# Optimization experiments

Measured on AMD Instinct MI355X. Metric: run time of the kernel, lower is better.

## Reference

```python
import jax, jax.numpy as jnp
import numpy as np

B, NS, NC, D = 32, 1024, 1024, 256   # batch, sentence len, comment len, latent/embedding dim
K = 128                              # co-attention latent size (self.k)
CLIP_R = 2.0
EPS = 1e-5

def _norm(x):
    return jnp.sqrt(jnp.maximum(jnp.sum(x * x, -1, keepdims=True), 1e-15))

def artanh(x):
    x = jnp.clip(x, -1 + 1e-5, 1 - 1e-5)
    return 0.5 * (jnp.log1p(x) - jnp.log1p(-x))

# ---------- Poincare ball, c = 1 ----------
def p_logmap0(y):
    yn = _norm(y)
    return artanh(yn) * y / yn

def p_expmap0(u):
    un = _norm(u)
    return jnp.tanh(un) * u / un

def mobius_add(x, y):
    xy = jnp.sum(x * y, -1, keepdims=True)
    x2 = jnp.sum(x * x, -1, keepdims=True)
    y2 = jnp.sum(y * y, -1, keepdims=True)
    num = (1 + 2 * xy + y2) * x + (1 - x2) * y
    den = jnp.maximum(1 + 2 * xy + x2 * y2, 1e-15)
    return num / den

def mobius_matvec(m, x):
    # geoopt convention: result = 'x @ m^T' transported through the ball
    xn = _norm(x)
    mx = jnp.matmul(x, jnp.swapaxes(m, -1, -2))
    mxn = _norm(mx)
    return jnp.tanh(mxn / xn * artanh(xn)) * mx / mxn

# ---------- Lorentz hyperboloid, k = 1 ----------
def l_expmap0_space(v_space):
    # exp map at origin of a tangent vector with zero time component
    vn = _norm(v_space)
    return jnp.concatenate([jnp.cosh(vn), jnp.sinh(vn) * v_space / vn], -1)

def euclid_to_lorentz(x):
    xn = _norm(x) + EPS
    x = x * jnp.minimum(1.0, CLIP_R / xn)  # clip_r feature clipping
    return l_expmap0_space(x)              # F.pad time=0 then expmap0

def lorentz_linear(x, W, b):
    y = jnp.matmul(x, W.T) + b
    space = y[..., 1:]
    time = jnp.sqrt(jnp.sum(space * space, -1, keepdims=True) + 1.0)
    return jnp.concatenate([time, space], -1)

def lorentz_act(x):
    space = jax.nn.gelu(x[..., 1:], approximate=False)
    time = jnp.sqrt(jnp.sum(space * space, -1, keepdims=True) + 1.0)
    return jnp.concatenate([time, space], -1)

def lorentz_to_poincare(x):
    return x[..., 1:] / (x[..., :1] + 1.0)

def l_inner(u, v):
    return -u[..., :1] * v[..., :1] + jnp.sum(u[..., 1:] * v[..., 1:], -1, keepdims=True)

def centroid(x, w):
    avg = jnp.matmul(w, x)  # weighted Lorentz average, then renormalize to hyperboloid
    den = jnp.sqrt(jnp.maximum(jnp.abs(l_inner(avg, avg)), 1e-8))
    return avg / den

def l_logmap0_space(x):
    t = jnp.maximum(x[..., :1], 1 + 1e-7)
    return jnp.arccosh(t) * x[..., 1:] / _norm(x[..., 1:])

def lorentz_concat(x, y):
    z = jnp.concatenate([l_logmap0_space(x), l_logmap0_space(y)], -1)
    return l_expmap0_space(z)


def setup_inputs() -> dict:
    key = jax.random.key(0)
    ks = jax.random.split(key, 8)
    sentence = jax.random.normal(ks[0], (B, NS, D), jnp.float32)
    comment = jax.random.normal(ks[1], (B, NC, D), jnp.float32)
    comment = 0.9 * comment / (_norm(comment) + 1.0)  # valid Poincare-ball points
    w = lambda k, o, i: jax.random.normal(k, (o, i), jnp.float32) * 0.05
    return {
        'sentence_rep': sentence,
        'comment_rep': comment,
        'Wl_W': w(ks[2], D + 1, D + 1), 'Wl_b': jnp.zeros((D + 1,), jnp.float32),
        'Wc_W': w(ks[3], K + 1, D + 1), 'Wc_b': jnp.zeros((K + 1,), jnp.float32),
        'Ws_W': w(ks[4], K + 1, D + 1), 'Ws_b': jnp.zeros((K + 1,), jnp.float32),
        'whs': jax.random.uniform(ks[5], (1, K), jnp.float32),
        'whc': jax.random.uniform(ks[6], (1, K), jnp.float32),
    }


def reference(sentence_rep, comment_rep, Wl_W, Wl_b, Wc_W, Wc_b, Ws_W, Ws_b, whs, whc):
    T = lambda a: jnp.swapaxes(a, -1, -2)
    # Fourier mixing (real part, as torch .float() on complex)
    s = jnp.fft.fft2(sentence_rep).real.astype(jnp.float32)
    c = jnp.fft.fft2(p_logmap0(comment_rep)).real.astype(jnp.float32)
    Ls = euclid_to_lorentz(s)            # [B,NS,D+1]
    Lc = euclid_to_lorentz(c)            # [B,NC,D+1]
    L = lorentz_linear(Lc, Wl_W, Wl_b)   # [B,NC,D+1]
    L = lorentz_act(jnp.einsum('bnd,bmd->bnm', Ls, L))  # [B,NS,NC] affinity
    # Ws(sentence) and Wc(comment) in Poincare coords (computed once; original recomputes)
    Hs_a = lorentz_to_poincare(lorentz_linear(Ls, Ws_W, Ws_b))  # [B,NS,K]
    Hc_a = lorentz_to_poincare(lorentz_linear(Lc, Wc_W, Wc_b))  # [B,NC,K]
    Hs_b = mobius_matvec(T(Hc_a), L)          # [B,NS,K]
    Hs = mobius_add(Hs_a, Hs_b)
    Hs = p_expmap0(jax.nn.gelu(p_logmap0(Hs), approximate=False))
    Hc_b = mobius_matvec(T(Hs_a), T(L))       # [B,NC,K]
    Hc = mobius_add(T(Hc_a), T(Hc_b))         # [B,K,NC]
    Hc = p_expmap0(jax.nn.gelu(p_logmap0(Hc), approximate=False))
    As = jax.nn.softmax(T(mobius_matvec(whs, Hs)), axis=-1)     # [B,1,NS]
    Ac = jax.nn.softmax(T(mobius_matvec(whc, T(Hc))), axis=-1)  # [B,1,NC]
    co_s = centroid(Ls, As)                   # [B,1,D+1]
    co_c = centroid(Lc, Ac)                   # [B,1,D+1]
    co_sc = jnp.squeeze(lorentz_concat(co_s, co_c), axis=1)     # [B,2D+1]
    return co_sc, As, Ac
```

## Files before the change

### kernel.cpp

```cpp
#include <hip/hip_runtime.h>
#include <cstdint>
#include <math.h>

#define NBATCH 32
#define NSQ 1024
#define NCQ 1024
#define DDIM 256
#define DP 257
#define KQ 128
#define KPAD 288
#define NFOLD 640
#define KF2 640
#define MXSPLIT 4194304

typedef __attribute__((ext_vector_type(8))) short short8;
typedef __attribute__((ext_vector_type(4))) float floatx4;

__device__ __forceinline__ float bf2f(ushort u) { return __uint_as_float(((uint)u) << 16); }
__device__ __forceinline__ ushort f2bf(float f) {
    uint u = __float_as_uint(f);
    return (ushort)((u + 0x7FFFu + ((u >> 16) & 1u)) >> 16);
}
__device__ __forceinline__ void gload16(const void* g, void* l) {
    __builtin_amdgcn_global_load_lds(
        (const __attribute__((address_space(1))) void*)g,
        (__attribute__((address_space(3))) void*)l,
        16, 0, 0);
}
__device__ __forceinline__ float artanh_clip(float x) {
    x = fminf(fmaxf(x, -1.0f + 1e-5f), 1.0f - 1e-5f);
    return 0.5f * (log1pf(x) - log1pf(-x));
}
__device__ __forceinline__ float gelu_f(float x) {
    return 0.5f * x * (1.0f + erff(x * 0.70710678118654752440f));
}
__device__ __forceinline__ float waveRedSum(float v) {
#pragma unroll
    for (int o = 32; o > 0; o >>= 1) v += __shfl_down(v, o, 64);
    return __shfl(v, 0, 64);
}
__device__ __forceinline__ void waveRedSum3(float& a, float& b, float& c) {
#pragma unroll
    for (int o = 32; o > 0; o >>= 1) {
        a += __shfl_down(a, o, 64);
        b += __shfl_down(b, o, 64);
        c += __shfl_down(c, o, 64);
    }
    a = __shfl(a, 0, 64); b = __shfl(b, 0, 64); c = __shfl(c, 0, 64);
}
__device__ __forceinline__ void waveRedSum2(float& a, float& b) {
#pragma unroll
    for (int o = 32; o > 0; o >>= 1) {
        a += __shfl_down(a, o, 64);
        b += __shfl_down(b, o, 64);
    }
    a = __shfl(a, 0, 64); b = __shfl(b, 0, 64);
}
__device__ __forceinline__ float blockRedSum(float v, float* buf) {
    int lane = threadIdx.x & 63, wid = threadIdx.x >> 6;
#pragma unroll
    for (int o = 32; o > 0; o >>= 1) v += __shfl_down(v, o, 64);
    __syncthreads();
    if (lane == 0) buf[wid] = v;
    __syncthreads();
    int nw = blockDim.x >> 6;
    float s = buf[0];
    for (int i = 1; i < nw; i++) s += buf[i];
    return s;
}
__device__ __forceinline__ float blockRedMax(float v, float* buf) {
    int lane = threadIdx.x & 63, wid = threadIdx.x >> 6;
#pragma unroll
    for (int o = 32; o > 0; o >>= 1) v = fmaxf(v, __shfl_down(v, o, 64));
    __syncthreads();
    if (lane == 0) buf[wid] = v;
    __syncthreads();
    int nw = blockDim.x >> 6;
    float s = buf[0];
    for (int i = 1; i < nw; i++) s = fmaxf(s, buf[i]);
    return s;
}

template <bool OUT_BF16, bool BIAS, bool ATOMIC, int NSPLIT, bool DUAL>
__global__ __launch_bounds__(256) void mfma_gemm(
    const short* __restrict__ A, int lda, int64_t sA,
    const short* __restrict__ B, int ldb, int64_t sB,
    void* __restrict__ Cv, int ldc, int64_t sC,
    const float* __restrict__ bias, int M, int N, int K,
    const short* __restrict__ A1, const short* __restrict__ B1, int64_t cOff1,
    const float* __restrict__ biasB)
{
    __shared__ short As0[128][32];
    __shared__ short Bs0[128][32];
    __shared__ short As1[128][32];
    __shared__ short Bs1[128][32];
    int bx = blockIdx.x, by = blockIdx.y, bz = blockIdx.z;
    {
        const int gx = gridDim.x, gy = gridDim.y;
        const int nblk = gx * gy * gridDim.z;
        if ((nblk & 7) == 0) {
            int flat = bx + gx * (by + gy * bz);
            int logical = (flat & 7) * (nblk >> 3) + (flat >> 3);
            bx = logical % gx; logical /= gx;
            by = logical % gy; bz = logical / gy;
        }
    }
    const int zz = bz;
    int zb, ks, half;
    if (DUAL) { half = zz & 1; zb = zz >> 1; ks = 0; }
    else      { zb = zz / NSPLIT; ks = zz - zb * NSPLIT; half = 0; }
    const short* Ap = (DUAL && half) ? A1 : A;
    const short* Bp = (DUAL && half) ? B1 : B;
    Ap += (int64_t)zb * sA;
    Bp += (int64_t)zb * sB;
    const int kper = K / NSPLIT;
    const int kbeg = ks * kper, kend = kbeg + kper;
    const int m0 = by * 128, n0 = bx * 128;
    const int t = threadIdx.x;
    const int lane = t & 63, w = t >> 6;
    const int wm = (w & 1) * 64, wn = (w >> 1) * 64;
    const int sr = t >> 2, sc8 = (t & 3) * 8;
    floatx4 acc[4][4] = {};

    auto stageA = [&](short (*S)[32], int kk) {
        const short* ap = Ap + (int64_t)(m0 + sr) * lda + kk + sc8;
        gload16(ap, &S[sr][sc8]);
        gload16(ap + (int64_t)64 * lda, &S[sr + 64][sc8]);
    };
    auto stageB = [&](short (*S)[32], int kk) {
        const short* bp = Bp + (int64_t)(n0 + sr) * ldb + kk + sc8;
        gload16(bp, &S[sr][sc8]);
        gload16(bp + (int64_t)64 * ldb, &S[sr + 64][sc8]);
    };
    auto domfma = [&](short (*SA)[32], short (*SB)[32]) {
        short8 af[4], bfv[4];
#pragma unroll
        for (int i = 0; i < 4; i++)
            af[i] = *(const short8*)&SA[wm + 16 * i + (lane & 15)][8 * (lane >> 4)];
#pragma unroll
        for (int i = 0; i < 4; i++)
            bfv[i] = *(const short8*)&SB[wn + 16 * i + (lane & 15)][8 * (lane >> 4)];
#pragma unroll
        for (int i = 0; i < 4; i++)
#pragma unroll
            for (int j = 0; j < 4; j++)
                acc[i][j] = __builtin_amdgcn_mfma_f32_16x16x32_bf16(af[i], bfv[j], acc[i][j], 0, 0, 0);
    };

    int k0 = kbeg;
    for (; k0 + 64 <= kend; k0 += 64) {
        stageA(As0, k0);       stageB(Bs0, k0);
        stageA(As1, k0 + 32);  stageB(Bs1, k0 + 32);
        __syncthreads();
        domfma(As0, Bs0);
        domfma(As1, Bs1);
        __syncthreads();
    }
    if (k0 < kend) {
        stageA(As0, k0);      stageB(Bs0, k0);
        __syncthreads();
        domfma(As0, Bs0);
        __syncthreads();
    }

    const int q = lane >> 4, c = lane & 15;
    int64_t cbase = (int64_t)zb * sC + ((DUAL && half) ? cOff1 : 0);
    if (NSPLIT > 1 && !ATOMIC) cbase += (int64_t)ks * cOff1;
    const float* bsel = (BIAS && biasB && zb) ? biasB : bias;
#pragma unroll
    for (int j = 0; j < 4; j++) {
        int col = n0 + wn + 16 * j + c;
        float bv = BIAS ? bsel[col] : 0.0f;
#pragma unroll
        for (int i = 0; i < 4; i++) {
            int rowb = m0 + wm + 16 * i + 4 * q;
#pragma unroll
            for (int r = 0; r < 4; r++) {
                float v = acc[i][j][r] + bv;
                int64_t idx = cbase + (int64_t)(rowb + r) * ldc + col;
                if (ATOMIC)       atomicAdd((float*)Cv + idx, v);
                else if (OUT_BF16) ((ushort*)Cv)[idx] = f2bf(v);
                else               ((float*)Cv)[idx] = v;
            }
        }
    }
}

__global__ __launch_bounds__(256) void trigtab_kernel(float* __restrict__ tab) {
    int p = blockIdx.x * 256 + threadIdx.x;
    float ang = (6.28318530717958647692f / 1024.0f) * (float)p;
    tab[p] = cosf(ang);
    tab[1024 + p] = sinf(ang);
}

__global__ __launch_bounds__(256) void genconst_kernel(
    const float* __restrict__ tab,
    ushort* CS1c, ushort* CS1s, ushort* C2, ushort* S2,
    const float* __restrict__ WlW, const float* __restrict__ WsW, const float* __restrict__ WcW,
    ushort* Wl, ushort* Ws, ushort* Wc)
{
    __shared__ float lct[1024], lst[1024];
    int blk = blockIdx.x, t = threadIdx.x;
    if (blk < 704) {
        for (int i = t; i < 1024; i += 256) { lct[i] = tab[i]; lst[i] = tab[1024 + i]; }
        __syncthreads();
    }
    if (blk < 640) {
        int n = blk;
        for (int k = t; k < 544; k += 256) {
            float vc, vs;
            if (k <= 512) {
                int p = (n * k) & 1023;
                vc = lct[p];
                vs = (k == 0) ? 0.0f : -lst[p];
            } else { vc = 0.0f; vs = 0.0f; }
            CS1c[n * KF2 + k] = f2bf(vc);
            CS1s[n * KF2 + k] = f2bf(vs);
        }
    } else if (blk < 704) {
        int base = (blk - 640) * 1024;
#pragma unroll
        for (int i = 0; i < 4; i++) {
            int idx = base + t + 256 * i;
            int d = idx >> 8, j = idx & 255;
            int p = ((d * j) & 255) << 2;
            C2[idx] = f2bf(lct[p]);
            S2[idx] = f2bf(lst[p]);
        }
    } else {
        int r = blk - 704;
        const float* src; ushort* dst; int srow;
        if (r < 256)      { src = WlW; dst = Wl + r * KPAD;        srow = r + 1; }
        else if (r < 384) { src = WsW; dst = Ws + (r - 256) * KPAD; srow = r - 256 + 1; }
        else              { src = WcW; dst = Wc + (r - 384) * KPAD; srow = r - 384 + 1; }
        dst[t] = (t < DP) ? f2bf(src[(int64_t)srow * DP + t]) : (ushort)0;
        if (t < KPAD - 256) {
            int t2 = t + 256;
            dst[t2] = (t2 < DP) ? f2bf(src[(int64_t)srow * DP + t2]) : (ushort)0;
        }
    }
}

__global__ __launch_bounds__(256) void prep_fold_kernel(const float* __restrict__ sent,
                                                        const float* __restrict__ comm,
                                                        ushort* __restrict__ XC, ushort* __restrict__ XS) {
    int bp = blockIdx.x;
    int z = blockIdx.y * 4 + (threadIdx.x >> 6);
    int lane = threadIdx.x & 63;
    int m2 = (1024 - bp) & 1023;
    const float* base = (z < 32) ? sent + (int64_t)z * 262144 : comm + (int64_t)(z - 32) * 262144;
    float4 a = *(const float4*)(base + bp * 256 + 4 * lane);
    float4 b = *(const float4*)(base + m2 * 256 + 4 * lane);
    if (z >= 32) {
        float s1 = a.x * a.x + a.y * a.y + a.z * a.z + a.w * a.w;
        float s2 = b.x * b.x + b.y * b.y + b.z * b.z + b.w * b.w;
        waveRedSum2(s1, s2);
        float yn1 = sqrtf(fmaxf(s1, 1e-15f));
        float f1 = artanh_clip(yn1) / yn1;
        a.x *= f1; a.y *= f1; a.z *= f1; a.w *= f1;
        float yn2 = sqrtf(fmaxf(s2, 1e-15f));
        float f2v = artanh_clip(yn2) / yn2;
        b.x *= f2v; b.y *= f2v; b.z *= f2v; b.w *= f2v;
    }
    int64_t o = ((int64_t)z * NFOLD + bp) * 256 + 4 * lane;
    bool single = (bp == 0) || (bp == 512);
    ushort4 oc;
    oc.x = f2bf(single ? a.x : a.x + b.x);
    oc.y = f2bf(single ? a.y : a.y + b.y);
    oc.z = f2bf(single ? a.z : a.z + b.z);
    oc.w = f2bf(single ? a.w : a.w + b.w);
    *(ushort4*)(XC + o) = oc;
    if (!single) {
        ushort4 os;
        os.x = f2bf(a.x - b.x); os.y = f2bf(a.y - b.y);
        os.z = f2bf(a.z - b.z); os.w = f2bf(a.w - b.w);
        *(ushort4*)(XS + o) = os;
    }
}

__global__ __launch_bounds__(256) void e2l_kernel(const ushort* __restrict__ YcYs,
                                                  ushort* __restrict__ Lsb, ushort* __restrict__ Lcb) {
    int64_t row = (int64_t)blockIdx.x * 4 + (threadIdx.x >> 6);
    int lane = threadIdx.x & 63;
    int z = (int)(row >> 10), n = (int)(row & 1023);
    int np = (n <= 512) ? n : 1024 - n;
    float sgn = (n <= 512) ? 1.0f : -1.0f;
    const ushort* base = YcYs + (int64_t)z * 327680 + np * 256 + 4 * lane;
    ushort4 uc = *(const ushort4*)base;
    ushort4 us = *(const ushort4*)(base + 163840);
    float v0 = bf2f(uc.x) + sgn * bf2f(us.x);
    float v1 = bf2f(uc.y) + sgn * bf2f(us.y);
    float v2 = bf2f(uc.z) + sgn * bf2f(us.z);
    float v3 = bf2f(uc.w) + sgn * bf2f(us.w);
    float s = waveRedSum(v0 * v0 + v1 * v1 + v2 * v2 + v3 * v3);
    float xn = sqrtf(fmaxf(s, 1e-15f)) + 1e-5f;
    float sc = fminf(1.0f, 2.0f / xn);
    float s2 = fmaxf(s * sc * sc, 1e-15f);
    float vn = sqrtf(s2);
    float e = expf(vn);
    float ei = 1.0f / e;
    float shv = (vn < 1e-4f) ? 1.0f : (e - ei) * 0.5f / vn;
    float fac = shv * sc;
    ushort* ob = (row < 32768 ? Lsb + row * KPAD : Lcb + (row - 32768) * KPAD);
    ob[1 + 4 * lane + 0] = f2bf(fac * v0);
    ob[1 + 4 * lane + 1] = f2bf(fac * v1);
    ob[1 + 4 * lane + 2] = f2bf(fac * v2);
    ob[1 + 4 * lane + 3] = f2bf(fac * v3);
    if (lane == 0) ob[0] = f2bf((e + ei) * 0.5f);
    if (lane < KPAD - DP) ob[DP + lane] = 0;
}

__global__ __launch_bounds__(256) void lnorm_kernel(ushort* __restrict__ Llin_bf) {
    int64_t row = (int64_t)blockIdx.x * 4 + (threadIdx.x >> 6);
    int lane = threadIdx.x & 63;
    ushort* ob = Llin_bf + row * KPAD;
    float s = 0.f;
#pragma unroll
    for (int i = 0; i < 4; i++) { float v = bf2f(ob[1 + 4 * lane + i]); s += v * v; }
    s = waveRedSum(s);
    if (lane == 0) ob[0] = f2bf(sqrtf(s + 1.0f));
    if (lane < KPAD - DP) ob[DP + lane] = 0;
}

__global__ __launch_bounds__(256) void poinc2_kernel(ushort* __restrict__ Hcat) {
    int64_t row = (int64_t)blockIdx.x * 4 + (threadIdx.x >> 6);
    int lane = threadIdx.x & 63;
    ushort* r = Hcat + row * KQ;
    ushort2 u = *(ushort2*)&r[2 * lane];
    float v0 = bf2f(u.x), v1 = bf2f(u.y);
    float s = waveRedSum(v0 * v0 + v1 * v1);
    float inv = 1.0f / (sqrtf(s + 1.0f) + 1.0f);
    ushort2 o; o.x = f2bf(v0 * inv); o.y = f2bf(v1 * inv);
    *(ushort2*)&r[2 * lane] = o;
}

__global__ __launch_bounds__(256) void tmat_kernel(ushort* __restrict__ inout, ushort* __restrict__ outp,
                                                   float* __restrict__ rowpart, float* __restrict__ colpart) {
    __shared__ ushort tile[64][68];
    int z = blockIdx.z;
    int r0 = blockIdx.x * 64, c0 = blockIdx.y * 64;
    ushort* ib = inout + (int64_t)z * 1048576;
    ushort* ob = outp + (int64_t)z * 1048576;
    int t = threadIdx.x;
    int row = t >> 2;
    int cq = (t & 3) * 8;
    {
        ushort* src = ib + (int64_t)(r0 + row) * 1024 + c0;
        float rsum = 0.f;
#pragma unroll
        for (int s = 0; s < 2; s++) {
            int cb = cq + 32 * s;
            uint4 v = *(const uint4*)(src + cb);
            ushort g[8];
            const ushort* pv = (const ushort*)&v;
#pragma unroll
            for (int k = 0; k < 8; k++) {
                g[k] = f2bf(gelu_f(bf2f(pv[k])));
                float fb = bf2f(g[k]);
                if (!(c0 == 0 && cb == 0 && k == 0)) rsum += fb * fb;
            }
            *(uint4*)(src + cb) = *(const uint4*)g;
            *(ushort4*)&tile[row][cb] = *(const ushort4*)&g[0];
            *(ushort4*)&tile[row][cb + 4] = *(const ushort4*)&g[4];
        }
        rsum += __shfl_xor(rsum, 1, 64);
        rsum += __shfl_xor(rsum, 2, 64);
        if ((t & 3) == 0)
            rowpart[((int64_t)(z * 16 + blockIdx.y)) * 1024 + r0 + row] = rsum;
    }
    __syncthreads();
    {
        int i2 = row;
        ushort* dst = ob + (int64_t)(c0 + i2) * 1024 + r0;
        float csum = 0.f;
#pragma unroll
        for (int s = 0; s < 2; s++) {
            int cb = cq + 32 * s;
            ushort g[8];
#pragma unroll
            for (int k = 0; k < 8; k++) {
                g[k] = tile[cb + k][i2];
                float a = bf2f(g[k]);
                csum += a * a;
            }
            *(uint4*)(dst + cb) = *(const uint4*)g;
        }
        csum += __shfl_xor(csum, 1, 64);
        csum += __shfl_xor(csum, 2, 64);
        if ((t & 3) == 0)
            colpart[((int64_t)(z * 16 + blockIdx.x)) * 1024 + c0 + i2] = csum;
    }
}

__global__ __launch_bounds__(256) void combine_kernel(
    const float* __restrict__ rowpart, const float* __restrict__ colpart,
    ushort* __restrict__ Lmat, ushort* __restrict__ LmatT,
    float* __restrict__ xnrow, float* __restrict__ colsum)
{
    __shared__ float red[4];
    int b = blockIdx.x, t = threadIdx.x;
    float t2 = 0.f;
#pragma unroll
    for (int i = 0; i < 4; i++) {
        int n = t + 256 * i;
        const float* rp = rowpart + (int64_t)b * 16384 + n;
        float s = 0.f;
#pragma unroll
        for (int c = 0; c < 16; c++) s += rp[c * 1024];
        float tim = sqrtf(1.0f + s);
        ushort tb = f2bf(tim);
        Lmat[((int64_t)(b * 1024 + n)) * 1024] = tb;
        LmatT[(int64_t)b * 1048576 + n] = tb;
        xnrow[b * 1024 + n] = sqrtf(fmaxf(1.0f + 2.0f * s, 1e-15f));
        t2 += tim * tim;
    }
#pragma unroll
    for (int i = 0; i < 4; i++) {
        int m = t + 256 * i;
        const float* cp = colpart + (int64_t)b * 16384 + m;
        float s = 0.f;
#pragma unroll
        for (int c = 0; c < 16; c++) s += cp[c * 1024];
        if (m > 0) colsum[b * 1024 + m] = s;
    }
    float tt = blockRedSum(t2, red);
    if (t == 0) colsum[b * 1024] = tt;
}

__global__ __launch_bounds__(256) void colfac_kernel(const float* __restrict__ colsum,
                                                     const float* __restrict__ mxcT,
                                                     float* __restrict__ fac_c) {
    int b = blockIdx.x; int m = blockIdx.y * 256 + threadIdx.x;
    float xn = sqrtf(fmaxf(colsum[b * NCQ + m], 1e-15f));
    const float* base = mxcT + (int64_t)b * KQ * NCQ + m;
    const float* base2 = base + MXSPLIT;
    float sm = 0.f;
    for (int j = 0; j < KQ; j++) {
        float v = base[j * NCQ] + base2[j * NCQ];
        sm += v * v;
    }
    float mxn = sqrtf(fmaxf(sm, 1e-15f));
    fac_c[b * NCQ + m] = tanhf(mxn / xn * artanh_clip(xn)) / mxn;
}

__global__ __launch_bounds__(256) void rowops_s_kernel(
    const ushort* __restrict__ Hsa, const float* __restrict__ mxs,
    const float* __restrict__ xnrow, const float* __restrict__ whs,
    float* __restrict__ logits)
{
    const int t = threadIdx.x;
    const int lane = t & 63;
    const int wid = t >> 6;
    const int sub = lane & 7;
    const int rg  = lane >> 3;
    const int64_t row = (int64_t)blockIdx.x * 32 + wid * 8 + rg;
    const ushort* p = Hsa + row * KQ + sub * 16;
    const float*  q = mxs + row * KQ + sub * 16;

    float pf[16], qf[16];
    {
        uint4 u0 = *(const uint4*)p;
        uint4 u1 = *(const uint4*)(p + 8);
        const ushort* pu0 = (const ushort*)&u0;
        const ushort* pu1 = (const ushort*)&u1;
#pragma unroll
        for (int i = 0; i < 8; i++) { pf[i] = bf2f(pu0[i]); pf[8 + i] = bf2f(pu1[i]); }
    }
#pragma unroll
    for (int i = 0; i < 16; i += 4) {
        float4 a  = *(const float4*)(q + i);
        float4 b2 = *(const float4*)(q + i + MXSPLIT);
        qf[i + 0] = a.x + b2.x; qf[i + 1] = a.y + b2.y;
        qf[i + 2] = a.z + b2.z; qf[i + 3] = a.w + b2.w;
    }
    float r1 = 0.f, r2 = 0.f, r3 = 0.f;
#pragma unroll
    for (int i = 0; i < 16; i++) {
        r1 += qf[i] * qf[i]; r2 += pf[i] * qf[i]; r3 += pf[i] * pf[i];
    }
#pragma unroll
    for (int o = 4; o > 0; o >>= 1) {
        r1 += __shfl_xor(r1, o, 64);
        r2 += __shfl_xor(r2, o, 64);
        r3 += __shfl_xor(r3, o, 64);
    }
    float mxn = sqrtf(fmaxf(r1, 1e-15f));
    float xn = xnrow[row];
    float fac = tanhf(mxn / xn * artanh_clip(xn)) / mxn;
    float xy = fac * r2;
    float x2 = r3;
    float y2 = fac * fac * r1;
    float ca = 1.f + 2.f * xy + y2, cb = 1.f - x2;
    float den = fmaxf(1.f + 2.f * xy + x2 * y2, 1e-15f);
    float hn2 = (ca * ca * x2 + 2.f * ca * cb * xy + cb * cb * y2) / (den * den);
    float hn = sqrtf(fmaxf(hn2, 1e-15f));
    float uf = artanh_clip(hn) / hn;
    float ufd = uf / den;
    float cbf = cb * fac;
    float wv[16];
#pragma unroll
    for (int i = 0; i < 16; i += 4) *(float4*)&wv[i] = *(const float4*)(whs + sub * 16 + i);
    float r4 = 0.f, r5 = 0.f;
#pragma unroll
    for (int i = 0; i < 16; i++) {
        float g = gelu_f(ufd * (ca * pf[i] + cbf * qf[i]));
        r4 += g * g;
        r5 += g * wv[i];
    }
#pragma unroll
    for (int o = 4; o > 0; o >>= 1) {
        r4 += __shfl_xor(r4, o, 64);
        r5 += __shfl_xor(r5, o, 64);
    }
    float gn = sqrtf(fmaxf(r4, 1e-15f));
    float ef = tanhf(gn) / gn;
    float dot = ef * r5;
    float Hn = sqrtf(fmaxf(ef * ef * r4, 1e-15f));
    float mxn2 = sqrtf(fmaxf(dot * dot, 1e-15f));
    float lg = tanhf(mxn2 / Hn * artanh_clip(Hn)) * dot / mxn2;
    if (sub == 0) logits[row] = lg;
}

__global__ void thsa_kernel(const ushort* __restrict__ in, ushort* __restrict__ outp) {
    __shared__ ushort tile[32][33];
    int z = blockIdx.z;
    int n0 = blockIdx.x * 32, j0 = blockIdx.y * 32;
    const ushort* ib = in + (int64_t)z * 131072;
    ushort* ob = outp + (int64_t)z * 131072;
    int tx = threadIdx.x, ty = threadIdx.y;
    for (int i = 0; i < 32; i += 8) tile[ty + i][tx] = ib[(n0 + ty + i) * 128 + j0 + tx];
    __syncthreads();
    for (int i = 0; i < 32; i += 8) ob[(j0 + ty + i) * 1024 + n0 + tx] = tile[tx][ty + i];
}

__global__ __launch_bounds__(256) void rowops_c_kernel(const ushort* __restrict__ HcAT,
                                                       float* __restrict__ mx,
                                                       const float* __restrict__ fac_c) {
    int64_t row = (int64_t)blockIdx.x * 4 + (threadIdx.x >> 6);
    int lane = threadIdx.x & 63;
    int b = (int)(row >> 7);
    const ushort* xb = HcAT + row * (int64_t)NCQ + 16 * lane;
    float* yb = mx + row * (int64_t)NCQ + 16 * lane;
    const float* fb = fac_c + b * NCQ + 16 * lane;
    float xv[16], yv[16];
    {
        uint4 u0 = *(const uint4*)xb;
        uint4 u1 = *(const uint4*)(xb + 8);
        const ushort* pu0 = (const ushort*)&u0;
        const ushort* pu1 = (const ushort*)&u1;
#pragma unroll
        for (int i = 0; i < 8; i++) { xv[i] = bf2f(pu0[i]); xv[8 + i] = bf2f(pu1[i]); }
    }
#pragma unroll
    for (int i = 0; i < 16; i += 4) {
        float4 v1 = *(const float4*)(yb + i);
        float4 v2 = *(const float4*)(yb + i + MXSPLIT);
        float4 fv = *(const float4*)(fb + i);
        yv[i + 0] = fv.x * (v1.x + v2.x);
        yv[i + 1] = fv.y * (v1.y + v2.y);
        yv[i + 2] = fv.z * (v1.z + v2.z);
        yv[i + 3] = fv.w * (v1.w + v2.w);
    }
    float xy = 0.f, x2 = 0.f, y2 = 0.f;
#pragma unroll
    for (int i = 0; i < 16; i++) { xy += xv[i] * yv[i]; x2 += xv[i] * xv[i]; y2 += yv[i] * yv[i]; }
    waveRedSum3(xy, x2, y2);
    float ca = 1.f + 2.f * xy + y2, cb = 1.f - x2;
    float den = fmaxf(1.f + 2.f * xy + x2 * y2, 1e-15f);
    float hn2 = (ca * ca * x2 + 2.f * ca * cb * xy + cb * cb * y2) / (den * den);
    float hn = sqrtf(fmaxf(hn2, 1e-15f));
    float uf = artanh_clip(hn) / hn;
    float g[16]; float gn2 = 0.f;
#pragma unroll
    for (int i = 0; i < 16; i++) {
        float h = (ca * xv[i] + cb * yv[i]) / den;
        g[i] = gelu_f(uf * h);
        gn2 += g[i] * g[i];
    }
    gn2 = waveRedSum(gn2);
    float gn = sqrtf(fmaxf(gn2, 1e-15f));
    float ef = tanhf(gn) / gn;
#pragma unroll
    for (int i = 0; i < 16; i += 4) {
        float4 o = {ef * g[i], ef * g[i + 1], ef * g[i + 2], ef * g[i + 3]};
        *(float4*)(yb + i) = o;
    }
}

__global__ __launch_bounds__(256) void logitsc_kernel(const float* __restrict__ Hc, const float* __restrict__ whc, float* __restrict__ lgc) {
    int b = blockIdx.x; int m = blockIdx.y * 256 + threadIdx.x;
    const float* base = Hc + (int64_t)b * KQ * NCQ + m;
    float s1 = 0.f, s2 = 0.f;
    for (int j = 0; j < KQ; j++) { float v = base[j * NCQ]; s1 += v * whc[j]; s2 += v * v; }
    float xn = sqrtf(fmaxf(s2, 1e-15f));
    float mxn = sqrtf(fmaxf(s1 * s1, 1e-15f));
    lgc[b * NCQ + m] = tanhf(mxn / xn * artanh_clip(xn)) * s1 / mxn;
}

__global__ __launch_bounds__(256) void softmax_kernel(const float* __restrict__ lg, float* __restrict__ outp) {
    __shared__ float red[4];
    int b = blockIdx.x; int t = threadIdx.x;
    const float* x = lg + b * 1024;
    float v[4]; float m = -1e30f;
#pragma unroll
    for (int i = 0; i < 4; i++) { v[i] = x[t + 256 * i]; m = fmaxf(m, v[i]); }
    m = blockRedMax(m, red);
    float s = 0.f;
#pragma unroll
    for (int i = 0; i < 4; i++) { v[i] = expf(v[i] - m); s += v[i]; }
    s = blockRedSum(s, red);
    float inv = 1.0f / s;
#pragma unroll
    for (int i = 0; i < 4; i++) outp[b * 1024 + t + 256 * i] = v[i] * inv;
}

__global__ __launch_bounds__(320) void centroidA_kernel(
    const ushort* __restrict__ Lsb, const ushort* __restrict__ Lcb,
    const float* __restrict__ As, const float* __restrict__ Ac,
    float* __restrict__ part)
{
    int b = blockIdx.x;
    int which = blockIdx.y;
    int chunk = blockIdx.z;
    const ushort* L = which ? Lcb : Lsb;
    const float* w = which ? Ac : As;
    int t = threadIdx.x;
    if (t >= DP) return;
    const ushort* Lb = L + (int64_t)b * NSQ * KPAD + (int64_t)chunk * 128 * KPAD + t;
    const float* wb = w + b * NSQ + chunk * 128;
    float s = 0.f;
    for (int n = 0; n < 128; n++) s += wb[n] * bf2f(Lb[(int64_t)n * KPAD]);
    part[((int64_t)((b * 2 + which) * 8 + chunk)) * 264 + t] = s;
}
__global__ __launch_bounds__(320) void centroidB_kernel(
    const float* __restrict__ part, float* __restrict__ co_s, float* __restrict__ co_c)
{
    int b = blockIdx.x;
    int which = blockIdx.y;
    int t = threadIdx.x;
    if (t >= DP) return;
    const float* p = part + (int64_t)(b * 2 + which) * 8 * 264 + t;
    float s = 0.f;
#pragma unroll
    for (int c = 0; c < 8; c++) s += p[c * 264];
    (which ? co_c : co_s)[b * DP + t] = s;
}

__global__ __launch_bounds__(256) void final_kernel(const float* __restrict__ co_s, const float* __restrict__ co_c, float* __restrict__ outp) {
    __shared__ float red[4];
    int b = blockIdx.x, t = threadIdx.x;
    float zmine[2];
    for (int w = 0; w < 2; w++) {
        const float* co = (w ? co_c : co_s) + b * DP;
        float at = co[0];
        float asp = co[1 + t];
        float ssp = blockRedSum(asp * asp, red);
        float li = ssp - at * at;
        float den = sqrtf(fmaxf(fabsf(li), 1e-8f));
        float xt = at / den, xsp = asp / den;
        float s2 = blockRedSum(xsp * xsp, red);
        float nrm = sqrtf(fmaxf(s2, 1e-15f));
        float ac = acoshf(fmaxf(xt, 1.0f + 1e-7f));
        zmine[w] = ac * xsp / nrm;
    }
    float vn2 = blockRedSum(zmine[0] * zmine[0] + zmine[1] * zmine[1], red);
    float vn = sqrtf(fmaxf(vn2, 1e-15f));
    float sc = sinhf(vn) / vn;
    if (t == 0) outp[b * 513] = coshf(vn);
    outp[b * 513 + 1 + t] = sc * zmine[0];
    outp[b * 513 + 1 + 256 + t] = sc * zmine[1];
}

extern "C" void kernel_launch(void* const* d_in, const int* in_sizes, int n_in,
                              void* d_out, int out_size, void* d_ws, size_t ws_size,
                              hipStream_t stream)
{
    const float* sent = (const float*)d_in[0];
    const float* comm = (const float*)d_in[1];
    const float* WlW  = (const float*)d_in[2];
    const float* Wlb  = (const float*)d_in[3];
    const float* WcW  = (const float*)d_in[4];
    const float* Wcb  = (const float*)d_in[5];
    const float* WsW  = (const float*)d_in[6];
    const float* Wsb  = (const float*)d_in[7];
    const float* whs  = (const float*)d_in[8];
    const float* whc  = (const float*)d_in[9];
    float* out = (float*)d_out;
    (void)in_sizes; (void)n_in; (void)out_size; (void)ws_size;

    float* ws = (float*)d_ws;
    size_t off = 0;
    auto take = [&](size_t n) { float* p = ws + off; off += n; return p; };
    float*  xnrow = take(32768);
    float*  fac_c = take(32768);
    float*  lgs   = take(32768);
    float*  lgc   = take(32768);
    float*  co_s  = take(8224);
    float*  co_c  = take(8224);
    float*  trigtab = take(2048);
    ushort* Ls_bf = (ushort*)take(4718592);
    ushort* Lc_bf = (ushort*)take(4718592);
    ushort* Wl_bf = (ushort*)take(36864);
    ushort* Ws_bf = (ushort*)take(18432);
    ushort* Wc_bf = (ushort*)take(18432);
    ushort* HsA_bf = (ushort*)take(2097152);
    ushort* HcA_bf = (ushort*)take(2097152);
    float*  part_cn   = take(1048576);
    float*  part_cent = take(135168);
    ushort* LmatT_bf  = (ushort*)take(16777216);
    float*  F     = take(33554432);

    ushort* XC_bf   = (ushort*)F;
    ushort* XS_bf   = (ushort*)(F + 5242880);
    ushort* Ff_bf   = (ushort*)(F + 10485760);
    ushort* CS1c    = (ushort*)(F + 20971520);
    ushort* CS1s    = (ushort*)(F + 21176320);
    ushort* C2_bf   = (ushort*)(F + 21381120);
    ushort* S2_bf   = (ushort*)(F + 21413888);
    ushort* YcYs    = (ushort*)F;
    ushort* Lmat_bf = (ushort*)F;
    ushort* Llin_bf = (ushort*)(F + 29360128);
    float*  mx      = F + 16777216;
    ushort* HsAT    = (ushort*)(F + 25165824);
    ushort* HcAT    = (ushort*)(F + 27262976);
    float*  colpart = F + 29360128;
    float*  colsum  = F + 30408704;

    float* AsOut = out + 16416;
    float* AcOut = out + 16416 + 32768;

    dim3 blk(256);
    const short* NUL = nullptr;

    trigtab_kernel<<<4, 256, 0, stream>>>(trigtab);
    genconst_kernel<<<1216, 256, 0, stream>>>(trigtab, CS1c, CS1s, C2_bf, S2_bf,
                                              WlW, WsW, WcW, Wl_bf, Ws_bf, Wc_bf);

    prep_fold_kernel<<<dim3(513, 16), blk, 0, stream>>>(sent, comm, XC_bf, XS_bf);
    mfma_gemm<true,false,false,1,true><<<dim3(5,2,128), blk, 0, stream>>>(
        (const short*)C2_bf,256,0, (const short*)XC_bf,256,(int64_t)NFOLD*256, Ff_bf,1280,(int64_t)256*1280,
        nullptr, 256,NFOLD,256, (const short*)S2_bf, (const short*)XS_bf, 640, nullptr);
    mfma_gemm<true,false,false,1,true><<<dim3(2,5,128), blk, 0, stream>>>(
        (const short*)CS1c,KF2,0, (const short*)Ff_bf,1280,(int64_t)256*1280, YcYs,256,327680,
        nullptr, NFOLD,256,544, (const short*)CS1s, (const short*)(Ff_bf+640), 163840, nullptr);
    e2l_kernel<<<16384, blk, 0, stream>>>(YcYs, Ls_bf, Lc_bf);

    mfma_gemm<true,true,false,1,false><<<dim3(2,256,1), blk, 0, stream>>>(
        (const short*)Lc_bf,KPAD,0, (const short*)Wl_bf,KPAD,0, (void*)(Llin_bf+1),KPAD,0,
        Wlb+1, 32768,256,KPAD, NUL, NUL, 0, nullptr);
    lnorm_kernel<<<8192, blk, 0, stream>>>(Llin_bf);

    mfma_gemm<true,false,false,1,false><<<dim3(8,8,32), blk, 0, stream>>>(
        (const short*)Ls_bf,KPAD,294912, (const short*)Llin_bf,KPAD,294912, Lmat_bf,1024,1048576,
        nullptr, 1024,1024,KPAD, NUL, NUL, 0, nullptr);
    tmat_kernel<<<dim3(16,16,32), blk, 0, stream>>>(Lmat_bf, LmatT_bf, part_cn, colpart);
    combine_kernel<<<32, blk, 0, stream>>>(part_cn, colpart, Lmat_bf, LmatT_bf, xnrow, colsum);

    mfma_gemm<true,true,false,1,false><<<dim3(1,256,2), blk, 0, stream>>>(
        (const short*)Ls_bf,KPAD,9437184, (const short*)Ws_bf,KPAD,36864, HsA_bf,128,4194304,
        Wsb+1, 32768,128,KPAD, NUL, NUL, 0, Wcb+1);
    poinc2_kernel<<<16384, blk, 0, stream>>>(HsA_bf);

    thsa_kernel<<<dim3(32,4,64), dim3(32,8), 0, stream>>>(HsA_bf, HsAT);

    mfma_gemm<false,false,false,2,false><<<dim3(1,8,64), blk, 0, stream>>>(
        (const short*)Lmat_bf,1024,1048576, (const short*)HcAT,1024,131072, mx,128,131072,
        nullptr, 1024,128,1024, NUL, NUL, MXSPLIT, nullptr);
    rowops_s_kernel<<<1024, blk, 0, stream>>>(HsA_bf, mx, xnrow, whs, lgs);

    mfma_gemm<false,false,false,2,false><<<dim3(8,1,64), blk, 0, stream>>>(
        (const short*)HsAT,1024,131072, (const short*)LmatT_bf,1024,1048576, mx,1024,131072,
        nullptr, 128,1024,1024, NUL, NUL, MXSPLIT, nullptr);
    colfac_kernel<<<dim3(32,4), blk, 0, stream>>>(colsum, mx, fac_c);
    rowops_c_kernel<<<1024, blk, 0, stream>>>(HcAT, mx, fac_c);
    logitsc_kernel<<<dim3(32,4), blk, 0, stream>>>(mx, whc, lgc);

    softmax_kernel<<<64, blk, 0, stream>>>(lgs, AsOut);
    centroidA_kernel<<<dim3(32,2,8), 320, 0, stream>>>(Ls_bf, Lc_bf, AsOut, AcOut, part_cent);
    centroidB_kernel<<<dim3(32,2), 320, 0, stream>>>(part_cent, co_s, co_c);
    final_kernel<<<32, blk, 0, stream>>>(co_s, co_c, out);
}
```

Baseline: 465.6 us.

## Fuse Poincare projection with transpose; simplify GEMM K-loop to single buffer

Merges the per-row Lorentz-to-Poincare normalization and the separate HsA transpose into one kernel. Each tile is read once, normalized, written back, and also written transposed through shared memory, which removes one launch and one global round trip. The MFMA GEMM main loop also changes from staging two 32-wide K chunks per barrier pair to one chunk per iteration with half the shared memory. That doubles the number of barriers per K step, which may hurt GEMM throughput but could raise occupancy.

Result: no change. 460.4 us (median of 3 runs) (-1.1%).

```diff
diff --git a/kernel.cpp b/kernel.cpp
--- a/kernel.cpp
+++ b/kernel.cpp
@@ -90,10 +90,8 @@
     const short* __restrict__ A1, const short* __restrict__ B1, int64_t cOff1,
     const float* __restrict__ biasB)
 {
-    __shared__ short As0[128][32];
-    __shared__ short Bs0[128][32];
-    __shared__ short As1[128][32];
-    __shared__ short Bs1[128][32];
+    __shared__ short As[128][32];
+    __shared__ short Bs[128][32];
     int bx = blockIdx.x, by = blockIdx.y, bz = blockIdx.z;
     {
         const int gx = gridDim.x, gy = gridDim.y;
@@ -119,50 +117,32 @@
     const int t = threadIdx.x;
     const int lane = t & 63, w = t >> 6;
     const int wm = (w & 1) * 64, wn = (w >> 1) * 64;
-    const int sr = t >> 2, sc8 = (t & 3) * 8;
     floatx4 acc[4][4] = {};
-
-    auto stageA = [&](short (*S)[32], int kk) {
-        const short* ap = Ap + (int64_t)(m0 + sr) * lda + kk + sc8;
-        gload16(ap, &S[sr][sc8]);
-        gload16(ap + (int64_t)64 * lda, &S[sr + 64][sc8]);
-    };
-    auto stageB = [&](short (*S)[32], int kk) {
-        const short* bp = Bp + (int64_t)(n0 + sr) * ldb + kk + sc8;
-        gload16(bp, &S[sr][sc8]);
-        gload16(bp + (int64_t)64 * ldb, &S[sr + 64][sc8]);
-    };
-    auto domfma = [&](short (*SA)[32], short (*SB)[32]) {
+    for (int k0 = kbeg; k0 < kend; k0 += 32) {
+        {
+            int r = t >> 2, c8 = (t & 3) * 8;
+            const short* ap = Ap + (int64_t)(m0 + r) * lda + k0 + c8;
+            gload16(ap, &As[r][c8]);
+            gload16(ap + (int64_t)64 * lda, &As[r + 64][c8]);
+            const short* bp = Bp + (int64_t)(n0 + r) * ldb + k0 + c8;
+            gload16(bp, &Bs[r][c8]);
+            gload16(bp + (int64_t)64 * ldb, &Bs[r + 64][c8]);
+        }
+        __syncthreads();
         short8 af[4], bfv[4];
 #pragma unroll
         for (int i = 0; i < 4; i++)
-            af[i] = *(const short8*)&SA[wm + 16 * i + (lane & 15)][8 * (lane >> 4)];
+            af[i] = *(const short8*)&As[wm + 16 * i + (lane & 15)][8 * (lane >> 4)];
 #pragma unroll
         for (int i = 0; i < 4; i++)
-            bfv[i] = *(const short8*)&SB[wn + 16 * i + (lane & 15)][8 * (lane >> 4)];
+            bfv[i] = *(const short8*)&Bs[wn + 16 * i + (lane & 15)][8 * (lane >> 4)];
 #pragma unroll
         for (int i = 0; i < 4; i++)
 #pragma unroll
             for (int j = 0; j < 4; j++)
                 acc[i][j] = __builtin_amdgcn_mfma_f32_16x16x32_bf16(af[i], bfv[j], acc[i][j], 0, 0, 0);
-    };
-
-    int k0 = kbeg;
-    for (; k0 + 64 <= kend; k0 += 64) {
-        stageA(As0, k0);       stageB(Bs0, k0);
-        stageA(As1, k0 + 32);  stageB(Bs1, k0 + 32);
         __syncthreads();
-        domfma(As0, Bs0);
-        domfma(As1, Bs1);
-        __syncthreads();
-    }
-    if (k0 < kend) {
-        stageA(As0, k0);      stageB(Bs0, k0);
-        __syncthreads();
-        domfma(As0, Bs0);
-        __syncthreads();
-    }
-
+    }
     const int q = lane >> 4, c = lane & 15;
     int64_t cbase = (int64_t)zb * sC + ((DUAL && half) ? cOff1 : 0);
     if (NSPLIT > 1 && !ATOMIC) cbase += (int64_t)ks * cOff1;
@@ -322,16 +302,54 @@
     if (lane < KPAD - DP) ob[DP + lane] = 0;
 }
 
-__global__ __launch_bounds__(256) void poinc2_kernel(ushort* __restrict__ Hcat) {
-    int64_t row = (int64_t)blockIdx.x * 4 + (threadIdx.x >> 6);
-    int lane = threadIdx.x & 63;
-    ushort* r = Hcat + row * KQ;
-    ushort2 u = *(ushort2*)&r[2 * lane];
-    float v0 = bf2f(u.x), v1 = bf2f(u.y);
-    float s = waveRedSum(v0 * v0 + v1 * v1);
-    float inv = 1.0f / (sqrtf(s + 1.0f) + 1.0f);
-    ushort2 o; o.x = f2bf(v0 * inv); o.y = f2bf(v1 * inv);
-    *(ushort2*)&r[2 * lane] = o;
+__global__ __launch_bounds__(256) void poincT_kernel(ushort* __restrict__ H, ushort* __restrict__ HT) {
+    __shared__ ushort tile[32][132];
+    int z = blockIdx.y;
+    int n0 = blockIdx.x * 32;
+    ushort* ib = H + (int64_t)z * 131072;
+    ushort* ob = HT + (int64_t)z * 131072;
+    int t = threadIdx.x;
+    {
+        int row = t >> 3;
+        int s0 = (t & 7) * 8;
+        ushort* src = ib + (int64_t)(n0 + row) * 128;
+        uint4 va = *(const uint4*)(src + s0);
+        uint4 vb = *(const uint4*)(src + s0 + 64);
+        float fa[8], fb[8];
+        const ushort* pa = (const ushort*)&va;
+        const ushort* pb = (const ushort*)&vb;
+        float s = 0.f;
+#pragma unroll
+        for (int i = 0; i < 8; i++) {
+            fa[i] = bf2f(pa[i]); fb[i] = bf2f(pb[i]);
+            s += fa[i] * fa[i] + fb[i] * fb[i];
+        }
+        s += __shfl_xor(s, 1, 64);
+        s += __shfl_xor(s, 2, 64);
+        s += __shfl_xor(s, 4, 64);
+        float inv = 1.0f / (sqrtf(s + 1.0f) + 1.0f);
+        ushort ga[8], gb[8];
+#pragma unroll
+        for (int i = 0; i < 8; i++) { ga[i] = f2bf(fa[i] * inv); gb[i] = f2bf(fb[i] * inv); }
+        *(uint4*)(src + s0) = *(const uint4*)ga;
+        *(uint4*)(src + s0 + 64) = *(const uint4*)gb;
+        *(ushort4*)&tile[row][s0] = *(const ushort4*)&ga[0];
+        *(ushort4*)&tile[row][s0 + 4] = *(const ushort4*)&ga[4];
+        *(ushort4*)&tile[row][s0 + 64] = *(const ushort4*)&gb[0];
+        *(ushort4*)&tile[row][s0 + 68] = *(const ushort4*)&gb[4];
+    }
+    __syncthreads();
+    {
+#pragma unroll
+        for (int p = 0; p < 2; p++) {
+            int j = p * 64 + (t >> 2);
+            int nq = (t & 3) * 8;
+            ushort g[8];
+#pragma unroll
+            for (int k = 0; k < 8; k++) g[k] = tile[nq + k][j];
+            *(uint4*)(ob + (int64_t)j * 1024 + n0 + nq) = *(const uint4*)g;
+        }
+    }
 }
 
 __global__ __launch_bounds__(256) void tmat_kernel(ushort* __restrict__ inout, ushort* __restrict__ outp,
@@ -519,18 +537,6 @@
     float mxn2 = sqrtf(fmaxf(dot * dot, 1e-15f));
     float lg = tanhf(mxn2 / Hn * artanh_clip(Hn)) * dot / mxn2;
     if (sub == 0) logits[row] = lg;
-}
-
-__global__ void thsa_kernel(const ushort* __restrict__ in, ushort* __restrict__ outp) {
-    __shared__ ushort tile[32][33];
-    int z = blockIdx.z;
-    int n0 = blockIdx.x * 32, j0 = blockIdx.y * 32;
-    const ushort* ib = in + (int64_t)z * 131072;
-    ushort* ob = outp + (int64_t)z * 131072;
-    int tx = threadIdx.x, ty = threadIdx.y;
-    for (int i = 0; i < 32; i += 8) tile[ty + i][tx] = ib[(n0 + ty + i) * 128 + j0 + tx];
-    __syncthreads();
-    for (int i = 0; i < 32; i += 8) ob[(j0 + ty + i) * 1024 + n0 + tx] = tile[tx][ty + i];
 }
 
 __global__ __launch_bounds__(256) void rowops_c_kernel(const ushort* __restrict__ HcAT,
@@ -759,9 +765,7 @@
     mfma_gemm<true,true,false,1,false><<<dim3(1,256,2), blk, 0, stream>>>(
         (const short*)Ls_bf,KPAD,9437184, (const short*)Ws_bf,KPAD,36864, HsA_bf,128,4194304,
         Wsb+1, 32768,128,KPAD, NUL, NUL, 0, Wcb+1);
-    poinc2_kernel<<<16384, blk, 0, stream>>>(HsA_bf);
-
-    thsa_kernel<<<dim3(32,4,64), dim3(32,8), 0, stream>>>(HsA_bf, HsAT);
+    poincT_kernel<<<dim3(32,64), blk, 0, stream>>>(HsA_bf, HsAT);
 
     mfma_gemm<false,false,false,2,false><<<dim3(1,8,64), blk, 0, stream>>>(
         (const short*)Lmat_bf,1024,1048576, (const short*)HcAT,1024,131072, mx,128,131072,
```
